# Performance work log

Measured on AMD Instinct MI355X. Metric: run time of the kernel, lower is better.

The kernel has to match this reference:

```python
import jax, jax.numpy as jnp
import numpy as np


def _lstm_layer(x, Wih, Whh, b):
    # torch nn.LSTM single layer, batch_first, gates in i,f,g,o order
    B, T, _ = x.shape
    H = Whh.shape[1]
    xg = jnp.einsum('btd,gd->btg', x, Wih) + b  # precompute input gates (B,T,4H)

    def step(carry, g_t):
        h, c = carry
        g = g_t + h @ Whh.T
        i, f, gg, o = jnp.split(g, 4, axis=-1)
        c = jax.nn.sigmoid(f) * c + jax.nn.sigmoid(i) * jnp.tanh(gg)
        h = jax.nn.sigmoid(o) * jnp.tanh(c)
        return (h, c), h

    z = jnp.zeros((B, H), x.dtype)
    _, hs = jax.lax.scan(step, (z, z), jnp.swapaxes(xg, 0, 1))
    return jnp.swapaxes(hs, 0, 1)


def _forward(x, x_lens, word_starts, word_ends, word_lens, tail_frames,
             fW_ih0, fW_hh0, fb0, fW_ih1, fW_hh1, fb1, fW_ih2, fW_hh2, fb2,
             fpW, fpb, wpW, wpb, lnW, lnB, wW_ih, wW_hh, wb, spW, spb):
    B, T, _ = x.shape
    # 3-layer frame LSTM (eval mode: inter-layer dropout disabled)
    h = _lstm_layer(x, fW_ih0, fW_hh0, fb0)
    h = _lstm_layer(h, fW_ih1, fW_hh1, fb1)
    h = _lstm_layer(h, fW_ih2, fW_hh2, fb2)
    # pad_packed_sequence zeros outputs beyond each sequence length
    tmask = (jnp.arange(T)[None, :] < x_lens[:, None]).astype(h.dtype)
    h = h * tmask[..., None]
    y_frame = h @ fpW.T + fpb  # (B,T,srv)

    # ragged per-word tail mean: r_j = mean h[i0:ef], i0 = max(ef-tail, sf)
    W = word_ends.shape[1]
    ef = jnp.minimum(word_ends, x_lens[:, None])
    sf = jnp.maximum(word_starts, 0)
    i0 = jnp.maximum(ef - tail_frames, sf)
    valid = ((jnp.arange(W)[None, :] < word_lens[:, None]) & (word_ends > 0)
             & (ef > sf) & (ef > i0))
    t = jnp.arange(T)
    m = (valid[:, :, None] & (t[None, None, :] >= i0[:, :, None])
         & (t[None, None, :] < ef[:, :, None])).astype(h.dtype)  # (B,W,T)
    cnt = jnp.maximum(m.sum(-1), 1.0)
    reps = jnp.einsum('bwt,bth->bwh', m, h) / cnt[..., None]  # (B,W,FH)

    # word_proj: Linear + LayerNorm + GELU (eval: dropout/noise/word-dropout off)
    r = reps @ wpW.T + wpb
    mu = r.mean(-1, keepdims=True)
    var = ((r - mu) ** 2).mean(-1, keepdims=True)
    r = (r - mu) / jnp.sqrt(var + 1e-5) * lnW + lnB
    r = jax.nn.gelu(r, approximate=False)

    lens = jnp.maximum(word_lens, 1)
    c = _lstm_layer(r, wW_ih, wW_hh, wb)
    wmask = (jnp.arange(W)[None, :] < lens[:, None]).astype(c.dtype)
    c = c * wmask[..., None]  # pad_packed(total_length=W) zeros
    pred_sem = c @ spW.T + spb  # (B,W,srv)
    return y_frame, x_lens, pred_sem


def setup_inputs() -> dict:
    key = jax.random.key(0)
    ks = jax.random.split(key, 24)
    B, T, D, SRV, FH, WR, WH, W = 16, 2000, 80, 512, 512, 256, 256, 100
    x = jax.random.normal(ks[0], (B, T, D), jnp.float32)
    x_lens = jax.random.randint(ks[1], (B,), T // 2, T + 1).at[0].set(T)
    ends = jnp.sort(jax.random.randint(ks[2], (B, W), 1, T + 1), axis=1)
    starts = jnp.concatenate([jnp.zeros((B, 1), ends.dtype), ends[:, :-1]], axis=1)
    word_lens = jax.random.randint(ks[3], (B,), 1, W + 1)

    def u(k, shape, fan):
        s = 1.0 / np.sqrt(fan)
        return jax.random.uniform(k, shape, jnp.float32, -s, s)

    return {
        'x': x, 'x_lens': x_lens, 'word_starts': starts, 'word_ends': ends,
        'word_lens': word_lens, 'tail_frames': 10,
        'fW_ih0': u(ks[4], (4 * FH, D), FH), 'fW_hh0': u(ks[5], (4 * FH, FH), FH), 'fb0': u(ks[6], (4 * FH,), FH),
        'fW_ih1': u(ks[7], (4 * FH, FH), FH), 'fW_hh1': u(ks[8], (4 * FH, FH), FH), 'fb1': u(ks[9], (4 * FH,), FH),
        'fW_ih2': u(ks[10], (4 * FH, FH), FH), 'fW_hh2': u(ks[11], (4 * FH, FH), FH), 'fb2': u(ks[12], (4 * FH,), FH),
        'fpW': u(ks[13], (SRV, FH), FH), 'fpb': u(ks[14], (SRV,), FH),
        'wpW': u(ks[15], (WR, FH), FH), 'wpb': u(ks[16], (WR,), FH),
        'lnW': jnp.ones((WR,), jnp.float32), 'lnB': jnp.zeros((WR,), jnp.float32),
        'wW_ih': u(ks[17], (4 * WH, WR), WH), 'wW_hh': u(ks[18], (4 * WH, WH), WH), 'wb': u(ks[19], (4 * WH,), WH),
        'spW': u(ks[20], (SRV, WH), WH), 'spb': u(ks[21], (SRV,), WH),
    }


def reference(x, x_lens, word_starts, word_ends, word_lens, tail_frames,
              fW_ih0, fW_hh0, fb0, fW_ih1, fW_hh1, fb1, fW_ih2, fW_hh2, fb2,
              fpW, fpb, wpW, wpb, lnW, lnB, wW_ih, wW_hh, wb, spW, spb):
    return _forward(x, x_lens, word_starts, word_ends, word_lens, tail_frames,
                    fW_ih0, fW_hh0, fb0, fW_ih1, fW_hh1, fb1, fW_ih2, fW_hh2, fb2,
                    fpW, fpb, wpW, wpb, lnW, lnB, wW_ih, wW_hh, wb, spW, spb)
```

## Files before the change

### kernel.cpp

```cpp
#include <hip/hip_runtime.h>
#include <math.h>

typedef unsigned short u16;
typedef unsigned int   u32;
typedef unsigned long long u64;
typedef __attribute__((ext_vector_type(8))) short short8;
typedef __attribute__((ext_vector_type(4))) float f32x4;

__device__ __forceinline__ float bf2f(u16 v) { return __uint_as_float(((u32)v) << 16); }
__device__ __forceinline__ u16 f2bf(float f) {
    u32 u = __float_as_uint(f);
    u32 r = (u + 0x7fffu + ((u >> 16) & 1u)) >> 16;
    return (u16)r;
}
__device__ __forceinline__ u32 pk2(float a, float b) {
    return ((u32)f2bf(a)) | (((u32)f2bf(b)) << 16);
}
__device__ __forceinline__ float sigm(float x) { return 1.f / (1.f + __expf(-x)); }
__device__ __forceinline__ f32x4 mfma16(short8 a, short8 b, f32x4 c) {
    return __builtin_amdgcn_mfma_f32_16x16x32_bf16(a, b, c, 0, 0, 0);
}
__device__ __forceinline__ short8 ld8bf(const float* p) {
    short8 r;
#pragma unroll
    for (int j = 0; j < 8; ++j) r[j] = (short)f2bf(p[j]);
    return r;
}
__device__ __forceinline__ short8 ldg16cv(const u16* p) {
    short8 r;
    asm volatile("global_load_dwordx4 %0, %1, off sc0 sc1" : "=v"(r) : "v"(p));
    return r;
}
__device__ __forceinline__ void waitvm() {
    asm volatile("s_waitcnt vmcnt(0)" ::: "memory");
}

#define FLAG_STRIDE 16
#define NPAR 8
#define BIGF (1 << 26)
#define XL_OFF 16384000
#define PS_OFF 16384016

#define WS_FLAGS   0
#define WS_HBUF_F  32768
#define WS_HBUF_W  425984
#define WS_REPS    491520
#define WS_RW      3768320
#define WS_HSEQ    4587520
#define WS_FPWB    6225920

template<int KTIN, bool L0>
__device__ __forceinline__ void frame_body(
    const int layer, const int kwg,
    const float* __restrict__ Wih, const float* __restrict__ Whh, const float* __restrict__ bias,
    const float* __restrict__ x, u16* __restrict__ hbuf, int* __restrict__ flags,
    float* __restrict__ h3out, float* sC, float* scs, u16* sxpad, u16* AsIn, u16* AsOwn)
{
    const int tid  = threadIdx.x;
    const int lane = tid & 63;
    const int wave = tid >> 6;
    const int n16  = lane & 15;
    const int quad = lane >> 4;
    const int koff = quad * 8;

    for (int e = tid; e < 144; e += 128) scs[e] = 0.f;
    if (L0) {
        for (int e = tid; e < 256; e += 128) sxpad[(e >> 4) * 96 + 80 + (e & 15)] = 0;
    }

    const int grow = wave * 1024 + ((n16 >> 3) * 512) + kwg * 8 + (n16 & 7);
    short8 bfr[KTIN + 16];
#pragma unroll
    for (int kt = 0; kt < KTIN; ++kt) {
        short8 v = {0,0,0,0,0,0,0,0};
        const int k = kt * 32 + koff;
        if (L0) { if (k + 8 <= 80) v = ld8bf(Wih + grow * 80 + k); }
        else    { v = ld8bf(Wih + (size_t)grow * 512 + k); }
        bfr[kt] = v;
    }
#pragma unroll
    for (int kt = 0; kt < 16; ++kt)
        bfr[KTIN + kt] = ld8bf(Whh + (size_t)grow * 512 + kt * 32 + koff);

    const int pb = (tid >> 4) & 3;
    const int cb = kwg * 8 + pb * 2;
    const float bI0 = bias[cb],        bI1 = bias[cb + 1];
    const float bF0 = bias[512 + cb],  bF1 = bias[512 + cb + 1];
    const float bG0 = bias[1024 + cb], bG1 = bias[1024 + cb + 1];
    const float bO0 = bias[1536 + cb], bO1 = bias[1536 + cb + 1];

    const int* fP = flags + (layer * 64) * FLAG_STRIDE;
    const int* fO = flags + ((layer + 1) * 64) * FLAG_STRIDE;
    const int* fN = flags + ((layer + 2) * 64) * FLAG_STRIDE;
    int* myflag   = flags + ((layer + 1) * 64 + kwg) * FLAG_STRIDE;
    __syncthreads();

    for (int t = 0; t < 2000; ++t) {
        if (wave == 0) {
            int guard = 0;
            for (;;) {
                const int fp = __hip_atomic_load(fP + lane * FLAG_STRIDE, __ATOMIC_RELAXED, __HIP_MEMORY_SCOPE_AGENT);
                const int fo = __hip_atomic_load(fO + lane * FLAG_STRIDE, __ATOMIC_RELAXED, __HIP_MEMORY_SCOPE_AGENT);
                const int fn = __hip_atomic_load(fN + lane * FLAG_STRIDE, __ATOMIC_RELAXED, __HIP_MEMORY_SCOPE_AGENT);
                if (__all((fp >= t + 1) && (fo >= t) && (fn >= t - 7))) break;
                if (++guard > (1 << 22)) break;
                __builtin_amdgcn_s_sleep(1);
            }
        }
        __syncthreads();

        const u16* hown = hbuf + ((size_t)(layer * NPAR + ((t + 7) & 7))) * 8192;
        short8 rin[8], rown[8];
        float4 xv0, xv1, xv2;
        if (L0) {
            const int e0 = tid, e1 = tid + 128, e2 = tid + 256;
            xv0 = *(const float4*)(x + ((size_t)(e0 / 20) * 2000 + t) * 80 + (e0 % 20) * 4);
            xv1 = *(const float4*)(x + ((size_t)(e1 / 20) * 2000 + t) * 80 + (e1 % 20) * 4);
            if (e2 < 320)
                xv2 = *(const float4*)(x + ((size_t)(e2 / 20) * 2000 + t) * 80 + (e2 % 20) * 4);
        } else {
            const u16* hin = hbuf + ((size_t)((layer - 1) * NPAR + (t & 7))) * 8192;
#pragma unroll
            for (int i = 0; i < 8; ++i) rin[i] = ldg16cv(hin + (tid + 128 * i) * 8);
        }
#pragma unroll
        for (int i = 0; i < 8; ++i) rown[i] = ldg16cv(hown + (tid + 128 * i) * 8);
        waitvm();
        if (L0) {
            const int e0 = tid, e1 = tid + 128, e2 = tid + 256;
            u32* d0 = (u32*)(sxpad + (e0 / 20) * 96 + (e0 % 20) * 4);
            d0[0] = pk2(xv0.x, xv0.y); d0[1] = pk2(xv0.z, xv0.w);
            u32* d1 = (u32*)(sxpad + (e1 / 20) * 96 + (e1 % 20) * 4);
            d1[0] = pk2(xv1.x, xv1.y); d1[1] = pk2(xv1.z, xv1.w);
            if (e2 < 320) {
                u32* d2 = (u32*)(sxpad + (e2 / 20) * 96 + (e2 % 20) * 4);
                d2[0] = pk2(xv2.x, xv2.y); d2[1] = pk2(xv2.z, xv2.w);
            }
        }
#pragma unroll
        for (int i = 0; i < 8; ++i) {
            const int c = tid + 128 * i;
            const int row = c >> 6, col8 = (c & 63) << 3;
            if (!L0) *(short8*)(AsIn + row * 520 + col8) = rin[i];
            *(short8*)(AsOwn + row * 520 + col8) = rown[i];
        }
        __syncthreads();

        f32x4 acc[4] = {{0,0,0,0},{0,0,0,0},{0,0,0,0},{0,0,0,0}};
#pragma unroll
        for (int kt = 0; kt < KTIN; ++kt) {
            short8 a;
            if (L0) a = *(const short8*)(sxpad + n16 * 96 + kt * 32 + koff);
            else    a = *(const short8*)(AsIn + n16 * 520 + kt * 32 + koff);
            acc[kt & 3] = mfma16(a, bfr[kt], acc[kt & 3]);
        }
#pragma unroll
        for (int kt = 0; kt < 16; ++kt) {
            short8 a = *(const short8*)(AsOwn + n16 * 520 + kt * 32 + koff);
            acc[(KTIN + kt) & 3] = mfma16(a, bfr[KTIN + kt], acc[(KTIN + kt) & 3]);
        }
        const f32x4 C = acc[0] + acc[1] + acc[2] + acc[3];
#pragma unroll
        for (int r = 0; r < 4; ++r)
            sC[(wave * 16 + quad * 4 + r) * 17 + n16] = C[r];
        __syncthreads();

        if (tid < 64) {
            const int b = tid & 15, p = tid >> 4;
            u32 pk = 0;
#pragma unroll
            for (int e = 0; e < 2; ++e) {
                const int jl = p * 2 + e;
                const float gi = sC[b * 17 + jl]             + (e ? bI1 : bI0);
                const float gf = sC[b * 17 + 8 + jl]         + (e ? bF1 : bF0);
                const float gg = sC[(16 + b) * 17 + jl]      + (e ? bG1 : bG0);
                const float go = sC[(16 + b) * 17 + 8 + jl]  + (e ? bO1 : bO0);
                const float cp = scs[b * 9 + jl];
                const float cn = sigm(gf) * cp + sigm(gi) * tanhf(gg);
                const float hn = sigm(go) * tanhf(cn);
                scs[b * 9 + jl] = cn;
                pk |= ((u32)f2bf(hn)) << (16 * e);
                if (!L0 && layer == 2)
                    h3out[((size_t)(b * 2000 + t)) * 512 + kwg * 8 + p * 2 + e] = hn;
            }
            u32* hdst = (u32*)(hbuf + ((size_t)(layer * NPAR + (t & 7))) * 8192 + b * 512 + kwg * 8 + p * 2);
            __hip_atomic_store(hdst, pk, __ATOMIC_RELAXED, __HIP_MEMORY_SCOPE_AGENT);
            waitvm();
            if (tid == 0)
                __hip_atomic_store(myflag, t + 1, __ATOMIC_RELAXED, __HIP_MEMORY_SCOPE_AGENT);
        }
    }
}

__global__ __launch_bounds__(128, 1) void k_frame_lstm(
    const float* __restrict__ x,
    const float* __restrict__ Wih0, const float* __restrict__ Whh0, const float* __restrict__ b0,
    const float* __restrict__ Wih1, const float* __restrict__ Whh1, const float* __restrict__ b1,
    const float* __restrict__ Wih2, const float* __restrict__ Whh2, const float* __restrict__ b2,
    u16* hbuf, int* flags, float* h3out)
{
    __shared__ __align__(16) u16 sxpad[16 * 96];
    __shared__ __align__(16) u16 AsIn[16 * 520];
    __shared__ __align__(16) u16 AsOwn[16 * 520];
    __shared__ float sC[32 * 17];
    __shared__ float scs[16 * 9];
    const int wgid = blockIdx.x;
    const int layer = wgid >> 6;
    const int kwg = wgid & 63;
    if (layer == 0)      frame_body<3,  true >(0, kwg, Wih0, Whh0, b0, x, hbuf, flags, h3out, sC, scs, sxpad, AsIn, AsOwn);
    else if (layer == 1) frame_body<16, false>(1, kwg, Wih1, Whh1, b1, x, hbuf, flags, h3out, sC, scs, sxpad, AsIn, AsOwn);
    else                 frame_body<16, false>(2, kwg, Wih2, Whh2, b2, x, hbuf, flags, h3out, sC, scs, sxpad, AsIn, AsOwn);
}

__global__ __launch_bounds__(128, 1) void k_word_lstm(
    const u16* __restrict__ rW, const float* __restrict__ Wih,
    const float* __restrict__ Whh, const float* __restrict__ bias,
    u16* __restrict__ hbufw, int* __restrict__ flags, float* __restrict__ hseq)
{
    __shared__ float sC[32 * 17];
    __shared__ float scs[16 * 9];
    const int tid = threadIdx.x;
    const int lane = tid & 63;
    const int wave = tid >> 6;
    const int n16 = lane & 15;
    const int quad = lane >> 4;
    const int koff = quad * 8;
    const int kwg = blockIdx.x;

    for (int e = tid; e < 144; e += 128) scs[e] = 0.f;
    const int grow = wave * 512 + ((n16 >> 3) * 256) + kwg * 8 + (n16 & 7);
    short8 bfr[16];
#pragma unroll
    for (int kt = 0; kt < 8; ++kt) bfr[kt]     = ld8bf(Wih + (size_t)grow * 256 + kt * 32 + koff);
#pragma unroll
    for (int kt = 0; kt < 8; ++kt) bfr[8 + kt] = ld8bf(Whh + (size_t)grow * 256 + kt * 32 + koff);
    const int pb = (tid >> 4) & 3;
    const int cb = kwg * 8 + pb * 2;
    const float bI0 = bias[cb],       bI1 = bias[cb + 1];
    const float bF0 = bias[256 + cb], bF1 = bias[256 + cb + 1];
    const float bG0 = bias[512 + cb], bG1 = bias[512 + cb + 1];
    const float bO0 = bias[768 + cb], bO1 = bias[768 + cb + 1];
    const int* fO = flags + 320 * FLAG_STRIDE;
    int* myflag   = flags + (320 + kwg) * FLAG_STRIDE;
    __syncthreads();
    const int aoff = n16 * 256 + koff;

    for (int t = 0; t < 100; ++t) {
        if (wave == 0) {
            int guard = 0;
            for (;;) {
                const int fo = (lane < 32)
                    ? __hip_atomic_load(fO + lane * FLAG_STRIDE, __ATOMIC_RELAXED, __HIP_MEMORY_SCOPE_AGENT)
                    : BIGF;
                if (__all(fo >= t)) break;
                if (++guard > (1 << 22)) break;
                __builtin_amdgcn_s_sleep(1);
            }
        }
        __syncthreads();
        const u16* hown = hbufw + ((size_t)((t + 7) & 7)) * 4096;
        short8 ha[8];
#pragma unroll
        for (int kt = 0; kt < 8; ++kt) ha[kt] = ldg16cv(hown + aoff + kt * 32);
        f32x4 acc[4] = {{0,0,0,0},{0,0,0,0},{0,0,0,0},{0,0,0,0}};
#pragma unroll
        for (int kt = 0; kt < 8; ++kt) {
            short8 a = *(const short8*)(rW + ((size_t)(n16 * 100 + t)) * 256 + koff + kt * 32);
            acc[kt & 3] = mfma16(a, bfr[kt], acc[kt & 3]);
        }
        waitvm();
#pragma unroll
        for (int kt = 0; kt < 8; ++kt)
            acc[kt & 3] = mfma16(ha[kt], bfr[8 + kt], acc[kt & 3]);
        const f32x4 C = acc[0] + acc[1] + acc[2] + acc[3];
#pragma unroll
        for (int r = 0; r < 4; ++r) sC[(wave * 16 + quad * 4 + r) * 17 + n16] = C[r];
        __syncthreads();
        if (tid < 64) {
            const int b = tid & 15, p = tid >> 4;
            u32 pk = 0;
#pragma unroll
            for (int e = 0; e < 2; ++e) {
                const int jl = p * 2 + e;
                const float gi = sC[b * 17 + jl]            + (e ? bI1 : bI0);
                const float gf = sC[b * 17 + 8 + jl]        + (e ? bF1 : bF0);
                const float gg = sC[(16 + b) * 17 + jl]     + (e ? bG1 : bG0);
                const float go = sC[(16 + b) * 17 + 8 + jl] + (e ? bO1 : bO0);
                const float cp = scs[b * 9 + jl];
                const float cn = sigm(gf) * cp + sigm(gi) * tanhf(gg);
                const float hn = sigm(go) * tanhf(cn);
                scs[b * 9 + jl] = cn;
                pk |= ((u32)f2bf(hn)) << (16 * e);
                hseq[((size_t)(b * 100 + t)) * 256 + kwg * 8 + p * 2 + e] = hn;
            }
            u32* hdst = (u32*)(hbufw + ((size_t)(t & 7)) * 4096 + b * 256 + kwg * 8 + p * 2);
            __hip_atomic_store(hdst, pk, __ATOMIC_RELAXED, __HIP_MEMORY_SCOPE_AGENT);
            waitvm();
            if (tid == 0)
                __hip_atomic_store(myflag, t + 1, __ATOMIC_RELAXED, __HIP_MEMORY_SCOPE_AGENT);
        }
    }
}

__global__ void k_pool(const float* __restrict__ h3, const int* __restrict__ x_lens,
                       const int* __restrict__ wstarts, const int* __restrict__ wends,
                       const int* __restrict__ wlens, const int* __restrict__ tailp,
                       float* __restrict__ reps)
{
    const int rw = blockIdx.x;
    const int b = rw / 100, w = rw - b * 100;
    const int tid = threadIdx.x;
    const int xl = x_lens[b];
    const int we = wends[rw];
    const int s0 = wstarts[rw];
    const int wl = wlens[b];
    const int tail = tailp[0];
    int ef = we < xl ? we : xl;
    int sf = s0 > 0 ? s0 : 0;
    int i0 = ef - tail; if (i0 < sf) i0 = sf;
    const bool valid = (w < wl) && (we > 0) && (ef > sf) && (ef > i0);
    float a0 = 0.f, a1 = 0.f;
    if (valid) {
        for (int t = i0; t < ef; ++t) {
            const float* hp = h3 + ((size_t)(b * 2000 + t)) * 512;
            a0 += hp[tid];
            a1 += hp[tid + 256];
        }
        const float inv = 1.f / (float)(ef - i0);
        a0 *= inv; a1 *= inv;
    }
    reps[(size_t)rw * 512 + tid] = a0;
    reps[(size_t)rw * 512 + tid + 256] = a1;
}

__global__ __launch_bounds__(256, 2) void k_frame_proj(
    float* __restrict__ y, const int* __restrict__ x_lens,
    const u16* __restrict__ fpWb, const float* __restrict__ fpb)
{
    __shared__ __align__(16) u16 As[16 * 520];
    const int tid = threadIdx.x, lane = tid & 63, wave = tid >> 6;
    const int n16 = lane & 15, quad = lane >> 4, koff = quad * 8;
    const int blk = blockIdx.x;
    const int b = blk / 125;
    const int t0 = (blk - b * 125) * 16;
    const int xl = x_lens[b];
    for (int c = tid; c < 2048; c += 256) {
        const int row = c >> 7;
        const int q = c & 127;
        const int t = t0 + row;
        float4 v = {0.f, 0.f, 0.f, 0.f};
        if (t < xl) v = *(const float4*)(y + ((size_t)(b * 2000 + t)) * 512 + q * 4);
        u32* d = (u32*)(As + row * 520 + q * 4);
        d[0] = pk2(v.x, v.y);
        d[1] = pk2(v.z, v.w);
    }
    __syncthreads();
    const size_t rowbase = (size_t)b * 2000 + t0;
    for (int ct = 0; ct < 8; ++ct) {
        const int col0 = (wave * 8 + ct) * 16;
        f32x4 acc = {0, 0, 0, 0};
#pragma unroll
        for (int kt = 0; kt < 16; ++kt) {
            short8 a = *(const short8*)(As + n16 * 520 + kt * 32 + koff);
            short8 wv = *(const short8*)(fpWb + ((size_t)(col0 + n16)) * 512 + kt * 32 + koff);
            acc = mfma16(a, wv, acc);
        }
        const float bn = fpb[col0 + n16];
#pragma unroll
        for (int r = 0; r < 4; ++r) {
            const int m = quad * 4 + r;
            y[(rowbase + m) * 512 + col0 + n16] = acc[r] + bn;
        }
    }
}

__global__ void k_word_proj(const float* __restrict__ reps, const float* __restrict__ wpW,
                            const float* __restrict__ wpb, const float* __restrict__ lnW,
                            const float* __restrict__ lnB, u16* __restrict__ rW)
{
    __shared__ float sx[512];
    __shared__ float red[512];
    const int tid = threadIdx.x;
    const int row = blockIdx.x;
    for (int k = tid; k < 512; k += 256) sx[k] = reps[(size_t)row * 512 + k];
    __syncthreads();
    float acc = wpb[tid];
    const float4* wr = (const float4*)(wpW + (size_t)tid * 512);
    for (int k4 = 0; k4 < 128; ++k4) {
        const float4 w = wr[k4];
        acc += sx[k4 * 4] * w.x + sx[k4 * 4 + 1] * w.y + sx[k4 * 4 + 2] * w.z + sx[k4 * 4 + 3] * w.w;
    }
    red[tid] = acc; red[256 + tid] = acc * acc;
    __syncthreads();
    for (int s = 128; s > 0; s >>= 1) {
        if (tid < s) { red[tid] += red[tid + s]; red[256 + tid] += red[256 + tid + s]; }
        __syncthreads();
    }
    const float mu = red[0] * (1.f / 256.f);
    float var = red[256] * (1.f / 256.f) - mu * mu;
    if (var < 0.f) var = 0.f;
    const float xn = (acc - mu) * rsqrtf(var + 1e-5f);
    const float yv = xn * lnW[tid] + lnB[tid];
    const float g = 0.5f * yv * (1.0f + erff(yv * 0.70710678118654752f));
    rW[(size_t)row * 256 + tid] = f2bf(g);
}

__global__ void k_pred(const float* __restrict__ hseq, const int* __restrict__ wlens,
                       const float* __restrict__ spW, const float* __restrict__ spb,
                       float* __restrict__ out)
{
    __shared__ float sh[256];
    const int tid = threadIdx.x;
    const int rw = blockIdx.x;
    const int b = rw / 100, w = rw - b * 100;
    int wl = wlens[b]; if (wl < 1) wl = 1;
    const bool valid = (w < wl);
    sh[tid] = valid ? hseq[(size_t)rw * 256 + tid] : 0.f;
    __syncthreads();
    for (int o = tid; o < 512; o += 256) {
        float acc = spb[o];
        const float4* wr = (const float4*)(spW + (size_t)o * 256);
        for (int k4 = 0; k4 < 64; ++k4) {
            const float4 wv = wr[k4];
            acc += sh[k4 * 4] * wv.x + sh[k4 * 4 + 1] * wv.y + sh[k4 * 4 + 2] * wv.z + sh[k4 * 4 + 3] * wv.w;
        }
        out[PS_OFF + (size_t)rw * 512 + o] = acc;
    }
}

__global__ void k_xlens(const int* __restrict__ x_lens, float* __restrict__ out)
{
    const int tid = threadIdx.x;
    if (tid < 16) out[XL_OFF + tid] = (float)x_lens[tid];
}

__global__ void k_cvt(const float* __restrict__ src, u16* __restrict__ dst)
{
    const int e = blockIdx.x * 256 + threadIdx.x;
    const float4 v = *(const float4*)(src + (size_t)e * 4);
    u32* d = (u32*)(dst + (size_t)e * 4);
    d[0] = pk2(v.x, v.y);
    d[1] = pk2(v.z, v.w);
}

__global__ void k_init(u32* __restrict__ p)
{
    const int idx = blockIdx.x * 256 + threadIdx.x;
    u32 v = 0u;
    if (idx < 8192) {
        const int slot = idx >> 4;
        if (slot < 64 || (slot >= 256 && slot < 320)) v = (u32)BIGF;
    }
    p[idx] = v;
}

extern "C" void kernel_launch(void* const* d_in, const int* in_sizes, int n_in,
                              void* d_out, int out_size, void* d_ws, size_t ws_size,
                              hipStream_t stream)
{
    (void)in_sizes; (void)n_in; (void)out_size; (void)ws_size;
    const float* x    = (const float*)d_in[0];
    const int* x_lens = (const int*)d_in[1];
    const int* wstart = (const int*)d_in[2];
    const int* wend   = (const int*)d_in[3];
    const int* wlen   = (const int*)d_in[4];
    const int* tailp  = (const int*)d_in[5];
    const float* Wih0 = (const float*)d_in[6];
    const float* Whh0 = (const float*)d_in[7];
    const float* b0   = (const float*)d_in[8];
    const float* Wih1 = (const float*)d_in[9];
    const float* Whh1 = (const float*)d_in[10];
    const float* b1   = (const float*)d_in[11];
    const float* Wih2 = (const float*)d_in[12];
    const float* Whh2 = (const float*)d_in[13];
    const float* b2   = (const float*)d_in[14];
    const float* fpW  = (const float*)d_in[15];
    const float* fpb  = (const float*)d_in[16];
    const float* wpW  = (const float*)d_in[17];
    const float* wpb  = (const float*)d_in[18];
    const float* lnW  = (const float*)d_in[19];
    const float* lnB  = (const float*)d_in[20];
    const float* wWih = (const float*)d_in[21];
    const float* wWhh = (const float*)d_in[22];
    const float* wb   = (const float*)d_in[23];
    const float* spW  = (const float*)d_in[24];
    const float* spb  = (const float*)d_in[25];

    float* out = (float*)d_out;
    char* ws = (char*)d_ws;
    int* flags  = (int*)(ws + WS_FLAGS);
    u16* hbufF  = (u16*)(ws + WS_HBUF_F);
    u16* hbufW  = (u16*)(ws + WS_HBUF_W);
    float* reps = (float*)(ws + WS_REPS);
    u16* rW     = (u16*)(ws + WS_RW);
    float* hseq = (float*)(ws + WS_HSEQ);
    u16* fpWb   = (u16*)(ws + WS_FPWB);

    k_init<<<480, 256, 0, stream>>>((u32*)d_ws);
    k_cvt<<<256, 256, 0, stream>>>(fpW, fpWb);
    k_frame_lstm<<<192, 128, 0, stream>>>(x, Wih0, Whh0, b0, Wih1, Whh1, b1,
                                          Wih2, Whh2, b2, hbufF, flags, out);
    k_pool<<<1600, 256, 0, stream>>>(out, x_lens, wstart, wend, wlen, tailp, reps);
    k_frame_proj<<<2000, 256, 0, stream>>>(out, x_lens, fpWb, fpb);
    k_word_proj<<<1600, 256, 0, stream>>>(reps, wpW, wpb, lnW, lnB, rW);
    k_word_lstm<<<32, 128, 0, stream>>>(rW, wWih, wWhh, wb, hbufW, flags, hseq);
    k_pred<<<1600, 256, 0, stream>>>(hseq, wlen, spW, spb, out);
    k_xlens<<<1, 64, 0, stream>>>(x_lens, out);
}
```

Before: 7.718 ms.

## Consolidate LSTM recurrence into fewer, wider workgroups with register cell state

The persistent frame LSTM moves from 64 workgroups of 128 threads per layer to 16 workgroups of 512 threads, each owning 32 hidden units. Word LSTM likewise goes from 32 to 8 workgroups. This cuts the number of flags polled per step and spreads the pointwise gate math across all threads, keeping the cell state in a register. The word LSTM also stages its inputs through LDS. Fewer, larger groups mean less cross-workgroup synchronisation per timestep but fewer CUs doing the recurrent matmul. Each group also does more LDS traffic and pays a heavier block barrier.

```diff
diff --git a/kernel.cpp b/kernel.cpp
--- a/kernel.cpp
+++ b/kernel.cpp
@@ -54,7 +54,7 @@
     const int layer, const int kwg,
     const float* __restrict__ Wih, const float* __restrict__ Whh, const float* __restrict__ bias,
     const float* __restrict__ x, u16* __restrict__ hbuf, int* __restrict__ flags,
-    float* __restrict__ h3out, float* sC, float* scs, u16* sxpad, u16* AsIn, u16* AsOwn)
+    float* __restrict__ h3out, float* sC, u16* sxpad, u16* AsIn, u16* AsOwn)
 {
     const int tid  = threadIdx.x;
     const int lane = tid & 63;
@@ -62,13 +62,14 @@
     const int n16  = lane & 15;
     const int quad = lane >> 4;
     const int koff = quad * 8;
-
-    for (int e = tid; e < 144; e += 128) scs[e] = 0.f;
+    const int gp   = wave >> 2;
+    const int cs   = wave & 3;
+
     if (L0) {
-        for (int e = tid; e < 256; e += 128) sxpad[(e >> 4) * 96 + 80 + (e & 15)] = 0;
-    }
-
-    const int grow = wave * 1024 + ((n16 >> 3) * 512) + kwg * 8 + (n16 & 7);
+        if (tid < 256) sxpad[(tid >> 4) * 96 + 80 + (tid & 15)] = 0;
+    }
+
+    const int grow = gp * 1024 + ((n16 >> 3) * 512) + kwg * 32 + cs * 8 + (n16 & 7);
     short8 bfr[KTIN + 16];
 #pragma unroll
     for (int kt = 0; kt < KTIN; ++kt) {
@@ -82,26 +83,28 @@
     for (int kt = 0; kt < 16; ++kt)
         bfr[KTIN + kt] = ld8bf(Whh + (size_t)grow * 512 + kt * 32 + koff);
 
-    const int pb = (tid >> 4) & 3;
-    const int cb = kwg * 8 + pb * 2;
-    const float bI0 = bias[cb],        bI1 = bias[cb + 1];
-    const float bF0 = bias[512 + cb],  bF1 = bias[512 + cb + 1];
-    const float bG0 = bias[1024 + cb], bG1 = bias[1024 + cb + 1];
-    const float bO0 = bias[1536 + cb], bO1 = bias[1536 + cb + 1];
-
-    const int* fP = flags + (layer * 64) * FLAG_STRIDE;
-    const int* fO = flags + ((layer + 1) * 64) * FLAG_STRIDE;
-    const int* fN = flags + ((layer + 2) * 64) * FLAG_STRIDE;
-    int* myflag   = flags + ((layer + 1) * 64 + kwg) * FLAG_STRIDE;
+    const int gb = tid & 15;
+    const int gj = tid >> 4;
+    const int gc = kwg * 32 + gj;
+    const float bI = bias[gc], bF = bias[512 + gc], bG = bias[1024 + gc], bO = bias[1536 + gc];
+    float creg = 0.f;
+
+    const int* fP = flags + (layer * 16) * FLAG_STRIDE;
+    const int* fO = flags + ((layer + 1) * 16) * FLAG_STRIDE;
+    const int* fN = flags + ((layer + 2) * 16) * FLAG_STRIDE;
+    int* myflag   = flags + ((layer + 1) * 16 + kwg) * FLAG_STRIDE;
+    const u16* pbase = hbuf + (size_t)((layer > 0 ? layer - 1 : 0) * NPAR) * 8192;
+    u16* lbase = hbuf + (size_t)(layer * NPAR) * 8192;
     __syncthreads();
 
     for (int t = 0; t < 2000; ++t) {
         if (wave == 0) {
+            const int idx = lane & 15;
             int guard = 0;
             for (;;) {
-                const int fp = __hip_atomic_load(fP + lane * FLAG_STRIDE, __ATOMIC_RELAXED, __HIP_MEMORY_SCOPE_AGENT);
-                const int fo = __hip_atomic_load(fO + lane * FLAG_STRIDE, __ATOMIC_RELAXED, __HIP_MEMORY_SCOPE_AGENT);
-                const int fn = __hip_atomic_load(fN + lane * FLAG_STRIDE, __ATOMIC_RELAXED, __HIP_MEMORY_SCOPE_AGENT);
+                const int fp = __hip_atomic_load(fP + idx * FLAG_STRIDE, __ATOMIC_RELAXED, __HIP_MEMORY_SCOPE_AGENT);
+                const int fo = __hip_atomic_load(fO + idx * FLAG_STRIDE, __ATOMIC_RELAXED, __HIP_MEMORY_SCOPE_AGENT);
+                const int fn = __hip_atomic_load(fN + idx * FLAG_STRIDE, __ATOMIC_RELAXED, __HIP_MEMORY_SCOPE_AGENT);
                 if (__all((fp >= t + 1) && (fo >= t) && (fn >= t - 7))) break;
                 if (++guard > (1 << 22)) break;
                 __builtin_amdgcn_s_sleep(1);
@@ -109,41 +112,32 @@
         }
         __syncthreads();
 
-        const u16* hown = hbuf + ((size_t)(layer * NPAR + ((t + 7) & 7))) * 8192;
-        short8 rin[8], rown[8];
-        float4 xv0, xv1, xv2;
+        const u16* hin  = pbase + ((size_t)(t & 7)) * 8192;
+        const u16* hown = lbase + ((size_t)((t + 7) & 7)) * 8192;
+        const int c0 = tid, c1 = tid + 512;
+        short8 rin0, rin1, rown0, rown1;
+        float4 xv;
         if (L0) {
-            const int e0 = tid, e1 = tid + 128, e2 = tid + 256;
-            xv0 = *(const float4*)(x + ((size_t)(e0 / 20) * 2000 + t) * 80 + (e0 % 20) * 4);
-            xv1 = *(const float4*)(x + ((size_t)(e1 / 20) * 2000 + t) * 80 + (e1 % 20) * 4);
-            if (e2 < 320)
-                xv2 = *(const float4*)(x + ((size_t)(e2 / 20) * 2000 + t) * 80 + (e2 % 20) * 4);
+            if (tid < 320)
+                xv = *(const float4*)(x + ((size_t)(tid / 20) * 2000 + t) * 80 + (tid % 20) * 4);
         } else {
-            const u16* hin = hbuf + ((size_t)((layer - 1) * NPAR + (t & 7))) * 8192;
-#pragma unroll
-            for (int i = 0; i < 8; ++i) rin[i] = ldg16cv(hin + (tid + 128 * i) * 8);
-        }
-#pragma unroll
-        for (int i = 0; i < 8; ++i) rown[i] = ldg16cv(hown + (tid + 128 * i) * 8);
+            rin0 = ldg16cv(hin + c0 * 8);
+            rin1 = ldg16cv(hin + c1 * 8);
+        }
+        rown0 = ldg16cv(hown + c0 * 8);
+        rown1 = ldg16cv(hown + c1 * 8);
         waitvm();
         if (L0) {
-            const int e0 = tid, e1 = tid + 128, e2 = tid + 256;
-            u32* d0 = (u32*)(sxpad + (e0 / 20) * 96 + (e0 % 20) * 4);
-            d0[0] = pk2(xv0.x, xv0.y); d0[1] = pk2(xv0.z, xv0.w);
-            u32* d1 = (u32*)(sxpad + (e1 / 20) * 96 + (e1 % 20) * 4);
-            d1[0] = pk2(xv1.x, xv1.y); d1[1] = pk2(xv1.z, xv1.w);
-            if (e2 < 320) {
-                u32* d2 = (u32*)(sxpad + (e2 / 20) * 96 + (e2 % 20) * 4);
-                d2[0] = pk2(xv2.x, xv2.y); d2[1] = pk2(xv2.z, xv2.w);
+            if (tid < 320) {
+                u32* d = (u32*)(sxpad + (tid / 20) * 96 + (tid % 20) * 4);
+                d[0] = pk2(xv.x, xv.y); d[1] = pk2(xv.z, xv.w);
             }
-        }
-#pragma unroll
-        for (int i = 0; i < 8; ++i) {
-            const int c = tid + 128 * i;
-            const int row = c >> 6, col8 = (c & 63) << 3;
-            if (!L0) *(short8*)(AsIn + row * 520 + col8) = rin[i];
-            *(short8*)(AsOwn + row * 520 + col8) = rown[i];
-        }
+        } else {
+            *(short8*)(AsIn + (c0 >> 6) * 520 + ((c0 & 63) << 3)) = rin0;
+            *(short8*)(AsIn + (c1 >> 6) * 520 + ((c1 & 63) << 3)) = rin1;
+        }
+        *(short8*)(AsOwn + (c0 >> 6) * 520 + ((c0 & 63) << 3)) = rown0;
+        *(short8*)(AsOwn + (c1 >> 6) * 520 + ((c1 & 63) << 3)) = rown1;
         __syncthreads();
 
         f32x4 acc[4] = {{0,0,0,0},{0,0,0,0},{0,0,0,0},{0,0,0,0}};
@@ -162,37 +156,33 @@
         const f32x4 C = acc[0] + acc[1] + acc[2] + acc[3];
 #pragma unroll
         for (int r = 0; r < 4; ++r)
-            sC[(wave * 16 + quad * 4 + r) * 17 + n16] = C[r];
-        __syncthreads();
-
-        if (tid < 64) {
-            const int b = tid & 15, p = tid >> 4;
-            u32 pk = 0;
-#pragma unroll
-            for (int e = 0; e < 2; ++e) {
-                const int jl = p * 2 + e;
-                const float gi = sC[b * 17 + jl]             + (e ? bI1 : bI0);
-                const float gf = sC[b * 17 + 8 + jl]         + (e ? bF1 : bF0);
-                const float gg = sC[(16 + b) * 17 + jl]      + (e ? bG1 : bG0);
-                const float go = sC[(16 + b) * 17 + 8 + jl]  + (e ? bO1 : bO0);
-                const float cp = scs[b * 9 + jl];
-                const float cn = sigm(gf) * cp + sigm(gi) * tanhf(gg);
-                const float hn = sigm(go) * tanhf(cn);
-                scs[b * 9 + jl] = cn;
-                pk |= ((u32)f2bf(hn)) << (16 * e);
-                if (!L0 && layer == 2)
-                    h3out[((size_t)(b * 2000 + t)) * 512 + kwg * 8 + p * 2 + e] = hn;
-            }
-            u32* hdst = (u32*)(hbuf + ((size_t)(layer * NPAR + (t & 7))) * 8192 + b * 512 + kwg * 8 + p * 2);
-            __hip_atomic_store(hdst, pk, __ATOMIC_RELAXED, __HIP_MEMORY_SCOPE_AGENT);
-            waitvm();
-            if (tid == 0)
-                __hip_atomic_store(myflag, t + 1, __ATOMIC_RELAXED, __HIP_MEMORY_SCOPE_AGENT);
-        }
-    }
-}
-
-__global__ __launch_bounds__(128, 1) void k_frame_lstm(
+            sC[(gp * 16 + quad * 4 + r) * 65 + cs * 16 + n16] = C[r];
+        __syncthreads();
+
+        const int cs2 = gj >> 3, jl = gj & 7;
+        const float gi = sC[gb * 65 + cs2 * 16 + jl]            + bI;
+        const float gf = sC[gb * 65 + cs2 * 16 + 8 + jl]        + bF;
+        const float gg = sC[(16 + gb) * 65 + cs2 * 16 + jl]     + bG;
+        const float go = sC[(16 + gb) * 65 + cs2 * 16 + 8 + jl] + bO;
+        const float cn = sigm(gf) * creg + sigm(gi) * tanhf(gg);
+        const float hn = sigm(go) * tanhf(cn);
+        creg = cn;
+        if (layer == 2)
+            h3out[((size_t)(gb * 2000 + t)) * 512 + gc] = hn;
+        const u32 mb = (u32)f2bf(hn);
+        const u32 nb = (u32)__shfl_xor((int)mb, 16, 64);
+        if (!(gj & 1)) {
+            u32* hd = (u32*)(lbase + ((size_t)(t & 7)) * 8192) + gb * 256 + kwg * 16 + (gj >> 1);
+            __hip_atomic_store(hd, mb | (nb << 16), __ATOMIC_RELAXED, __HIP_MEMORY_SCOPE_AGENT);
+        }
+        waitvm();
+        __syncthreads();
+        if (tid == 0)
+            __hip_atomic_store(myflag, t + 1, __ATOMIC_RELAXED, __HIP_MEMORY_SCOPE_AGENT);
+    }
+}
+
+__global__ __launch_bounds__(512, 1) void k_frame_lstm(
     const float* __restrict__ x,
     const float* __restrict__ Wih0, const float* __restrict__ Whh0, const float* __restrict__ b0,
     const float* __restrict__ Wih1, const float* __restrict__ Whh1, const float* __restrict__ b1,
@@ -202,103 +192,106 @@
     __shared__ __align__(16) u16 sxpad[16 * 96];
     __shared__ __align__(16) u16 AsIn[16 * 520];
     __shared__ __align__(16) u16 AsOwn[16 * 520];
-    __shared__ float sC[32 * 17];
-    __shared__ float scs[16 * 9];
+    __shared__ float sC[32 * 65];
     const int wgid = blockIdx.x;
-    const int layer = wgid >> 6;
-    const int kwg = wgid & 63;
-    if (layer == 0)      frame_body<3,  true >(0, kwg, Wih0, Whh0, b0, x, hbuf, flags, h3out, sC, scs, sxpad, AsIn, AsOwn);
-    else if (layer == 1) frame_body<16, false>(1, kwg, Wih1, Whh1, b1, x, hbuf, flags, h3out, sC, scs, sxpad, AsIn, AsOwn);
-    else                 frame_body<16, false>(2, kwg, Wih2, Whh2, b2, x, hbuf, flags, h3out, sC, scs, sxpad, AsIn, AsOwn);
-}
-
-__global__ __launch_bounds__(128, 1) void k_word_lstm(
+    const int layer = wgid >> 4;
+    const int kwg = wgid & 15;
+    if (layer == 0)      frame_body<3,  true >(0, kwg, Wih0, Whh0, b0, x, hbuf, flags, h3out, sC, sxpad, AsIn, AsOwn);
+    else if (layer == 1) frame_body<16, false>(1, kwg, Wih1, Whh1, b1, x, hbuf, flags, h3out, sC, sxpad, AsIn, AsOwn);
+    else                 frame_body<16, false>(2, kwg, Wih2, Whh2, b2, x, hbuf, flags, h3out, sC, sxpad, AsIn, AsOwn);
+}
+
+__global__ __launch_bounds__(512, 1) void k_word_lstm(
     const u16* __restrict__ rW, const float* __restrict__ Wih,
     const float* __restrict__ Whh, const float* __restrict__ bias,
     u16* __restrict__ hbufw, int* __restrict__ flags, float* __restrict__ hseq)
 {
-    __shared__ float sC[32 * 17];
-    __shared__ float scs[16 * 9];
+    __shared__ __align__(16) u16 AsIn[16 * 264];
+    __shared__ __align__(16) u16 AsOwn[16 * 264];
+    __shared__ float sC[32 * 65];
     const int tid = threadIdx.x;
     const int lane = tid & 63;
     const int wave = tid >> 6;
     const int n16 = lane & 15;
     const int quad = lane >> 4;
     const int koff = quad * 8;
+    const int gp = wave >> 2;
+    const int cs = wave & 3;
     const int kwg = blockIdx.x;
 
-    for (int e = tid; e < 144; e += 128) scs[e] = 0.f;
-    const int grow = wave * 512 + ((n16 >> 3) * 256) + kwg * 8 + (n16 & 7);
+    const int grow = gp * 512 + ((n16 >> 3) * 256) + kwg * 32 + cs * 8 + (n16 & 7);
     short8 bfr[16];
 #pragma unroll
     for (int kt = 0; kt < 8; ++kt) bfr[kt]     = ld8bf(Wih + (size_t)grow * 256 + kt * 32 + koff);
 #pragma unroll
     for (int kt = 0; kt < 8; ++kt) bfr[8 + kt] = ld8bf(Whh + (size_t)grow * 256 + kt * 32 + koff);
-    const int pb = (tid >> 4) & 3;
-    const int cb = kwg * 8 + pb * 2;
-    const float bI0 = bias[cb],       bI1 = bias[cb + 1];
-    const float bF0 = bias[256 + cb], bF1 = bias[256 + cb + 1];
-    const float bG0 = bias[512 + cb], bG1 = bias[512 + cb + 1];
-    const float bO0 = bias[768 + cb], bO1 = bias[768 + cb + 1];
-    const int* fO = flags + 320 * FLAG_STRIDE;
-    int* myflag   = flags + (320 + kwg) * FLAG_STRIDE;
+    const int gb = tid & 15;
+    const int gj = tid >> 4;
+    const int gc = kwg * 32 + gj;
+    const float bI = bias[gc], bF = bias[256 + gc], bG = bias[512 + gc], bO = bias[768 + gc];
+    float creg = 0.f;
+    const int* fO = flags + 80 * FLAG_STRIDE;
+    int* myflag   = flags + (80 + kwg) * FLAG_STRIDE;
     __syncthreads();
-    const int aoff = n16 * 256 + koff;
 
     for (int t = 0; t < 100; ++t) {
         if (wave == 0) {
+            const int idx = lane & 7;
             int guard = 0;
             for (;;) {
-                const int fo = (lane < 32)
-                    ? __hip_atomic_load(fO + lane * FLAG_STRIDE, __ATOMIC_RELAXED, __HIP_MEMORY_SCOPE_AGENT)
-                    : BIGF;
+                const int fo = __hip_atomic_load(fO + idx * FLAG_STRIDE, __ATOMIC_RELAXED, __HIP_MEMORY_SCOPE_AGENT);
                 if (__all(fo >= t)) break;
                 if (++guard > (1 << 22)) break;
                 __builtin_amdgcn_s_sleep(1);
             }
         }
         __syncthreads();
+
         const u16* hown = hbufw + ((size_t)((t + 7) & 7)) * 4096;
-        short8 ha[8];
-#pragma unroll
-        for (int kt = 0; kt < 8; ++kt) ha[kt] = ldg16cv(hown + aoff + kt * 32);
+        const int b = tid >> 5, k8 = (tid & 31) << 3;
+        const short8 rv = *(const short8*)(rW + ((size_t)(b * 100 + t)) * 256 + k8);
+        const short8 hv = ldg16cv(hown + tid * 8);
+        waitvm();
+        *(short8*)(AsIn + b * 264 + k8) = rv;
+        *(short8*)(AsOwn + b * 264 + k8) = hv;
+        __syncthreads();
+
         f32x4 acc[4] = {{0,0,0,0},{0,0,0,0},{0,0,0,0},{0,0,0,0}};
 #pragma unroll
         for (int kt = 0; kt < 8; ++kt) {
-            short8 a = *(const short8*)(rW + ((size_t)(n16 * 100 + t)) * 256 + koff + kt * 32);
+            short8 a = *(const short8*)(AsIn + n16 * 264 + kt * 32 + koff);
             acc[kt & 3] = mfma16(a, bfr[kt], acc[kt & 3]);
         }
+#pragma unroll
+        for (int kt = 0; kt < 8; ++kt) {
+            short8 a = *(const short8*)(AsOwn + n16 * 264 + kt * 32 + koff);
+            acc[kt & 3] = mfma16(a, bfr[8 + kt], acc[kt & 3]);
+        }
+        const f32x4 C = acc[0] + acc[1] + acc[2] + acc[3];
+#pragma unroll
+        for (int r = 0; r < 4; ++r)
+            sC[(gp * 16 + quad * 4 + r) * 65 + cs * 16 + n16] = C[r];
+        __syncthreads();
+
+        const int cs2 = gj >> 3, jl = gj & 7;
+        const float gi = sC[gb * 65 + cs2 * 16 + jl]            + bI;
+        const float gf = sC[gb * 65 + cs2 * 16 + 8 + jl]        + bF;
+        const float gg = sC[(16 + gb) * 65 + cs2 * 16 + jl]     + bG;
+        const float go = sC[(16 + gb) * 65 + cs2 * 16 + 8 + jl] + bO;
+        const float cn = sigm(gf) * creg + sigm(gi) * tanhf(gg);
+        const float hn = sigm(go) * tanhf(cn);
+        creg = cn;
+        hseq[((size_t)(gb * 100 + t)) * 256 + gc] = hn;
+        const u32 mb = (u32)f2bf(hn);
+        const u32 nb = (u32)__shfl_xor((int)mb, 16, 64);
+        if (!(gj & 1)) {
+            u32* hd = (u32*)(hbufw + ((size_t)(t & 7)) * 4096) + gb * 128 + kwg * 16 + (gj >> 1);
+            __hip_atomic_store(hd, mb | (nb << 16), __ATOMIC_RELAXED, __HIP_MEMORY_SCOPE_AGENT);
+        }
         waitvm();
-#pragma unroll
-        for (int kt = 0; kt < 8; ++kt)
-            acc[kt & 3] = mfma16(ha[kt], bfr[8 + kt], acc[kt & 3]);
-        const f32x4 C = acc[0] + acc[1] + acc[2] + acc[3];
-#pragma unroll
-        for (int r = 0; r < 4; ++r) sC[(wave * 16 + quad * 4 + r) * 17 + n16] = C[r];
-        __syncthreads();
-        if (tid < 64) {
-            const int b = tid & 15, p = tid >> 4;
-            u32 pk = 0;
-#pragma unroll
-            for (int e = 0; e < 2; ++e) {
-                const int jl = p * 2 + e;
-                const float gi = sC[b * 17 + jl]            + (e ? bI1 : bI0);
-                const float gf = sC[b * 17 + 8 + jl]        + (e ? bF1 : bF0);
-                const float gg = sC[(16 + b) * 17 + jl]     + (e ? bG1 : bG0);
-                const float go = sC[(16 + b) * 17 + 8 + jl] + (e ? bO1 : bO0);
-                const float cp = scs[b * 9 + jl];
-                const float cn = sigm(gf) * cp + sigm(gi) * tanhf(gg);
-                const float hn = sigm(go) * tanhf(cn);
-                scs[b * 9 + jl] = cn;
-                pk |= ((u32)f2bf(hn)) << (16 * e);
-                hseq[((size_t)(b * 100 + t)) * 256 + kwg * 8 + p * 2 + e] = hn;
-            }
-            u32* hdst = (u32*)(hbufw + ((size_t)(t & 7)) * 4096 + b * 256 + kwg * 8 + p * 2);
-            __hip_atomic_store(hdst, pk, __ATOMIC_RELAXED, __HIP_MEMORY_SCOPE_AGENT);
-            waitvm();
-            if (tid == 0)
-                __hip_atomic_store(myflag, t + 1, __ATOMIC_RELAXED, __HIP_MEMORY_SCOPE_AGENT);
-        }
+        __syncthreads();
+        if (tid == 0)
+            __hip_atomic_store(myflag, t + 1, __ATOMIC_RELAXED, __HIP_MEMORY_SCOPE_AGENT);
     }
 }
 
@@ -449,7 +442,7 @@
     u32 v = 0u;
     if (idx < 8192) {
         const int slot = idx >> 4;
-        if (slot < 64 || (slot >= 256 && slot < 320)) v = (u32)BIGF;
+        if (slot < 16 || (slot >= 64 && slot < 80)) v = (u32)BIGF;
     }
     p[idx] = v;
 }
@@ -498,12 +491,12 @@
 
     k_init<<<480, 256, 0, stream>>>((u32*)d_ws);
     k_cvt<<<256, 256, 0, stream>>>(fpW, fpWb);
-    k_frame_lstm<<<192, 128, 0, stream>>>(x, Wih0, Whh0, b0, Wih1, Whh1, b1,
-                                          Wih2, Whh2, b2, hbufF, flags, out);
+    k_frame_lstm<<<48, 512, 0, stream>>>(x, Wih0, Whh0, b0, Wih1, Whh1, b1,
+                                         Wih2, Whh2, b2, hbufF, flags, out);
     k_pool<<<1600, 256, 0, stream>>>(out, x_lens, wstart, wend, wlen, tailp, reps);
     k_frame_proj<<<2000, 256, 0, stream>>>(out, x_lens, fpWb, fpb);
     k_word_proj<<<1600, 256, 0, stream>>>(reps, wpW, wpb, lnW, lnB, rW);
-    k_word_lstm<<<32, 128, 0, stream>>>(rW, wWih, wWhh, wb, hbufW, flags, hseq);
+    k_word_lstm<<<8, 512, 0, stream>>>(rW, wWih, wWhh, wb, hbufW, flags, hseq);
     k_pred<<<1600, 256, 0, stream>>>(hseq, wlen, spW, spb, out);
     k_xlens<<<1, 64, 0, stream>>>(x_lens, out);
 }
```

Result: slower. 8.175 ms (+5.9%).
